# Kernel tuning notes

Hardware: AMD Instinct MI355X
Metric: run time of the kernel (lower is better)

The kernel has to match this reference:

```python
import jax, jax.numpy as jnp
import numpy as np

N_NODES = 25000
N_EDGES = 250000
DIM = 64
HEADS = 4
BN_EPS = 1e-5


def setup_inputs() -> dict:
    key = jax.random.key(0)
    ks = jax.random.split(key, 6)
    x = jax.random.normal(ks[0], (N_NODES, DIM), dtype=jnp.float32)
    edge_index = jax.random.randint(ks[1], (2, N_EDGES), 0, N_NODES)
    edge_attr = jax.random.normal(ks[2], (N_EDGES, DIM), dtype=jnp.float32)
    # learned params of GATGNN_AGAT_LAYER (xavier-ish scale)
    W = jax.random.normal(ks[3], (2 * DIM, HEADS * DIM), dtype=jnp.float32) * 0.05
    att = jax.random.normal(ks[4], (1, HEADS, 2 * DIM), dtype=jnp.float32) * 0.05
    bias = jnp.zeros((DIM,), dtype=jnp.float32)
    # BatchNorm1d(heads) in eval mode (running stats)
    bn_gamma = jnp.ones((HEADS,), dtype=jnp.float32)
    bn_beta = jnp.zeros((HEADS,), dtype=jnp.float32)
    bn_mean = jnp.zeros((HEADS,), dtype=jnp.float32)
    bn_var = jnp.ones((HEADS,), dtype=jnp.float32)
    return {"x": x, "edge_attr": edge_attr, "W": W, "att": att, "bias": bias,
            "bn_gamma": bn_gamma, "bn_beta": bn_beta, "bn_mean": bn_mean,
            "bn_var": bn_var, "edge_index": edge_index}


def reference(x, edge_attr, W, att, bias, bn_gamma, bn_beta, bn_mean, bn_var, edge_index):
    act = jax.nn.softplus  # act='softplus' in DSDCrystal
    # flow='target_to_source': i = edge_index[0] (aggregation index), j = edge_index[1]
    idx_i = edge_index[0]
    idx_j = edge_index[1]
    x_i = x[idx_i]                                   # [E, D] gather
    x_j = x[idx_j]                                   # [E, D] gather
    out_i = act(jnp.concatenate([x_i, edge_attr], axis=-1) @ W)  # [E, H*D]
    out_j = act(jnp.concatenate([x_j, edge_attr], axis=-1) @ W)  # [E, H*D]
    out_i = out_i.reshape(-1, HEADS, DIM)            # [E, H, D]
    out_j = out_j.reshape(-1, HEADS, DIM)
    # multi-head attention logits
    alpha = act(jnp.sum(jnp.concatenate([out_i, out_j], axis=-1) * att, axis=-1))  # [E, H]
    # BatchNorm1d(heads), eval mode
    alpha = act((alpha - bn_mean) / jnp.sqrt(bn_var + BN_EPS) * bn_gamma + bn_beta)
    # segment softmax over edges sharing the same target node i
    amax = jax.ops.segment_max(alpha, idx_i, num_segments=N_NODES)  # [N, H]
    e = jnp.exp(alpha - amax[idx_i])
    denom = jax.ops.segment_sum(e, idx_i, num_segments=N_NODES)[idx_i]  # [E, H]
    alpha = e / denom
    # weighted messages, scatter-add aggregation (dropout p=0.0 / eval)
    msg = out_j * alpha[:, :, None]                  # [E, H, D]
    aggr = jax.ops.segment_sum(msg, idx_i, num_segments=N_NODES)  # [N, H, D]
    # update: mean over heads + bias
    return aggr.mean(axis=1) + bias                  # [N, D]
```

## Files before the change

### kernel.cpp

```cpp
#include <hip/hip_runtime.h>
#include <hip/hip_bf16.h>
#include <math.h>

#define NN 25000
#define NE 250000
#define DD 64
#define HH 4
#define NGROUP (NE / 16)
#define NB 98

typedef __attribute__((ext_vector_type(8))) short bf16x8;
typedef __attribute__((ext_vector_type(4))) float f32x4;

#define WT_LD 136

__device__ __forceinline__ float softplus_f(float x) {
    return fmaxf(x, 0.0f) + __logf(1.0f + __expf(-fabsf(x)));
}

__device__ __forceinline__ unsigned short f2bf(float f) {
    __hip_bfloat16 h = __float2bfloat16(f);
    unsigned short u;
    __builtin_memcpy(&u, &h, 2);
    return u;
}

__device__ __forceinline__ float bf2f(unsigned short u) {
    return __uint_as_float(((unsigned int)u) << 16);
}

__device__ __forceinline__ void load8(const float* p, bf16x8& hi, bf16x8& lo) {
    float4 a = *(const float4*)p;
    float4 b = *(const float4*)(p + 4);
    float v[8] = {a.x, a.y, a.z, a.w, b.x, b.y, b.z, b.w};
#pragma unroll
    for (int i = 0; i < 8; ++i) {
        unsigned short h = f2bf(v[i]);
        hi[i] = (short)h;
        lo[i] = (short)f2bf(v[i] - bf2f(h));
    }
}

__global__ __launch_bounds__(512, 4)
void k_edge(const float* __restrict__ x, const float* __restrict__ ea,
            const float* __restrict__ W, const float* __restrict__ att,
            const float* __restrict__ bn_g, const float* __restrict__ bn_b,
            const float* __restrict__ bn_m, const float* __restrict__ bn_v,
            const int* __restrict__ eidx,
            unsigned short* __restrict__ outj,
            float* __restrict__ expa, float* __restrict__ denom)
{
    __shared__ unsigned short Wsh[256 * WT_LD];
    __shared__ float attI[256], attJ[256];

    const int tid = threadIdx.x;
    const int lane = tid & 63;
    const int q = lane >> 4;
    const int r = lane & 15;

    for (int idx = tid; idx < 32768; idx += 512) {
        int k = idx >> 8, n = idx & 255;
        Wsh[n * WT_LD + k] = f2bf(W[idx]);
    }
    if (tid < 256) {
        int c = tid;
        attI[c] = att[(c >> 6) * 128 + (c & 63)];
        attJ[c] = att[(c >> 6) * 128 + 64 + (c & 63)];
    }
    float bnsc[HH], bnsh[HH];
#pragma unroll
    for (int t = 0; t < HH; ++t) {
        float inv = rsqrtf(bn_v[t] + 1e-5f);
        bnsc[t] = bn_g[t] * inv;
        bnsh[t] = bn_b[t] - bn_m[t] * bn_g[t] * inv;
    }
    __syncthreads();

    const int gw = blockIdx.x * 8 + (tid >> 6);
    const int nw = gridDim.x * 8;

    for (int g = gw; g < NGROUP; g += nw) {
        const int e0 = g * 16;
        const int ei = eidx[e0 + r];
        const int ej = eidx[NE + e0 + r];
        const float* xi = x + (size_t)ei * DD;
        const float* xj = x + (size_t)ej * DD;
        const float* ev = ea + (size_t)(e0 + r) * DD;

        bf16x8 Ahi[6], Alo[6];
        load8(xi + q * 8,      Ahi[0], Alo[0]);
        load8(xi + 32 + q * 8, Ahi[1], Alo[1]);
        load8(xj + q * 8,      Ahi[2], Alo[2]);
        load8(xj + 32 + q * 8, Ahi[3], Alo[3]);
        load8(ev + q * 8,      Ahi[4], Alo[4]);
        load8(ev + 32 + q * 8, Ahi[5], Alo[5]);

        float lg[4][4];
#pragma unroll
        for (int a = 0; a < 4; ++a)
#pragma unroll
            for (int b = 0; b < 4; ++b) lg[a][b] = 0.f;

#pragma unroll
        for (int nt = 0; nt < 4; ++nt) {
            f32x4 ai[4], aj[4];
#pragma unroll
            for (int h = 0; h < 4; ++h) {
                ai[h] = (f32x4){0.f, 0.f, 0.f, 0.f};
                aj[h] = (f32x4){0.f, 0.f, 0.f, 0.f};
            }
#pragma unroll
            for (int h = 0; h < 4; ++h) {
                const unsigned short* bp = &Wsh[((nt + 4 * h) * 16 + r) * WT_LD + q * 8];
#pragma unroll
                for (int kt = 0; kt < 4; ++kt) {
                    bf16x8 bf = *(const bf16x8*)(bp + kt * 32);
                    const int fi = (kt < 2) ? kt : kt + 2;
                    const int fj = kt + 2;
                    ai[h] = __builtin_amdgcn_mfma_f32_16x16x32_bf16(Ahi[fi], bf, ai[h], 0, 0, 0);
                    ai[h] = __builtin_amdgcn_mfma_f32_16x16x32_bf16(Alo[fi], bf, ai[h], 0, 0, 0);
                    aj[h] = __builtin_amdgcn_mfma_f32_16x16x32_bf16(Ahi[fj], bf, aj[h], 0, 0, 0);
                    aj[h] = __builtin_amdgcn_mfma_f32_16x16x32_bf16(Alo[fj], bf, aj[h], 0, 0, 0);
                }
            }
            const int dbase = nt * 16 + r;
#pragma unroll
            for (int reg = 0; reg < 4; ++reg) {
                ushort4 pk;
                unsigned short* pkp = (unsigned short*)&pk;
#pragma unroll
                for (int h = 0; h < 4; ++h) {
                    const int c = dbase + 64 * h;
                    float spi = softplus_f(ai[h][reg]);
                    float spj = softplus_f(aj[h][reg]);
                    lg[reg][h] += spi * attI[c] + spj * attJ[c];
                    pkp[h] = f2bf(spj);
                }
                const unsigned e = (unsigned)(e0 + q * 4 + reg);
                *(ushort4*)&outj[e * 256 + dbase * 4] = pk;
            }
        }

#pragma unroll
        for (int off = 1; off < 16; off <<= 1) {
#pragma unroll
            for (int a = 0; a < 4; ++a)
#pragma unroll
                for (int b = 0; b < 4; ++b)
                    lg[a][b] += __shfl_xor(lg[a][b], off, 64);
        }
        float exv[4][4];
#pragma unroll
        for (int reg = 0; reg < 4; ++reg)
#pragma unroll
            for (int h = 0; h < 4; ++h)
                exv[reg][h] = __expf(softplus_f(fmaf(lg[reg][h], bnsc[h], bnsh[h])));

        if (r < 4) {
#pragma unroll
            for (int reg = 0; reg < 4; ++reg) {
                const int e = e0 + q * 4 + reg;
                const int ii = eidx[e];
                expa[e * 4 + r] = exv[reg][r];
                atomicAdd(&denom[ii * 4 + r], exv[reg][r]);
            }
        }
    }
}

__global__ __launch_bounds__(256)
void k_hist(const int* __restrict__ eidx, int* __restrict__ cnt) {
    const int e = blockIdx.x * 256 + threadIdx.x;
    if (e < NE) atomicAdd(&cnt[eidx[e]], 1);
}

__global__ __launch_bounds__(256)
void k_scanA(const int* __restrict__ cnt, int* __restrict__ offs,
             int* __restrict__ bsum) {
    __shared__ int s[256];
    const int tid = threadIdx.x;
    const int i = blockIdx.x * 256 + tid;
    int v = (i < NN) ? cnt[i] : 0;
    s[tid] = v;
    __syncthreads();
#pragma unroll
    for (int off = 1; off < 256; off <<= 1) {
        int t = (tid >= off) ? s[tid - off] : 0;
        __syncthreads();
        s[tid] += t;
        __syncthreads();
    }
    if (i < NN) offs[i] = s[tid] - v;
    if (tid == 255) bsum[blockIdx.x] = s[255];
}

__global__ __launch_bounds__(128)
void k_scanB(const int* __restrict__ bsum, int* __restrict__ bbase) {
    __shared__ int s[128];
    const int tid = threadIdx.x;
    int v = (tid < NB) ? bsum[tid] : 0;
    s[tid] = v;
    __syncthreads();
#pragma unroll
    for (int off = 1; off < 128; off <<= 1) {
        int t = (tid >= off) ? s[tid - off] : 0;
        __syncthreads();
        s[tid] += t;
        __syncthreads();
    }
    if (tid < NB) bbase[tid] = s[tid] - v;
}

__global__ __launch_bounds__(256)
void k_scanC(int* __restrict__ offs, const int* __restrict__ bbase,
             int* __restrict__ cursor) {
    const int i = blockIdx.x * 256 + threadIdx.x;
    if (i < NN) {
        const int o = offs[i] + bbase[blockIdx.x];
        offs[i] = o;
        cursor[i] = o;
    }
    if (i == 0) offs[NN] = NE;
}

__global__ __launch_bounds__(256)
void k_place(const int* __restrict__ eidx, int* __restrict__ cursor,
             int* __restrict__ perm) {
    const int e = blockIdx.x * 256 + threadIdx.x;
    if (e < NE) {
        const int pos = atomicAdd(&cursor[eidx[e]], 1);
        perm[pos] = e;
    }
}

__global__ __launch_bounds__(256)
void k_aggr(const int* __restrict__ offs, const int* __restrict__ perm,
            const unsigned short* __restrict__ outj,
            const float* __restrict__ expa,
            const float* __restrict__ denom,
            const float* __restrict__ bias,
            float* __restrict__ out)
{
    const int n = blockIdx.x * 4 + (threadIdx.x >> 6);
    if (n >= NN) return;
    const int lane = threadIdx.x & 63;
    const int k0 = offs[n], k1 = offs[n + 1];
    const float4 dv = *(const float4*)&denom[n * 4];
    float num0 = 0.f, num1 = 0.f, num2 = 0.f, num3 = 0.f;

    if (k0 < k1) {
        int e = perm[k0];
        float4 ex = *(const float4*)&expa[e * 4];
        ushort4 v = *(const ushort4*)&outj[((unsigned)e << 8) | (lane << 2)];
        for (int k = k0; k < k1; ++k) {
            float4 exc = ex; ushort4 vc = v;
            if (k + 1 < k1) {
                const int e2 = perm[k + 1];
                ex = *(const float4*)&expa[e2 * 4];
                v  = *(const ushort4*)&outj[((unsigned)e2 << 8) | (lane << 2)];
            }
            num0 += exc.x * bf2f(vc.x);
            num1 += exc.y * bf2f(vc.y);
            num2 += exc.z * bf2f(vc.z);
            num3 += exc.w * bf2f(vc.w);
        }
    }
    float r = 0.f;
    r += (dv.x > 0.f) ? num0 / dv.x : 0.f;
    r += (dv.y > 0.f) ? num1 / dv.y : 0.f;
    r += (dv.z > 0.f) ? num2 / dv.z : 0.f;
    r += (dv.w > 0.f) ? num3 / dv.w : 0.f;
    out[n * DD + lane] = 0.25f * r + bias[lane];
}

extern "C" void kernel_launch(void* const* d_in, const int* in_sizes, int n_in,
                              void* d_out, int out_size, void* d_ws, size_t ws_size,
                              hipStream_t stream)
{
    (void)in_sizes; (void)n_in; (void)out_size; (void)ws_size;
    const float* x    = (const float*)d_in[0];
    const float* ea   = (const float*)d_in[1];
    const float* W    = (const float*)d_in[2];
    const float* att  = (const float*)d_in[3];
    const float* bias = (const float*)d_in[4];
    const float* bn_g = (const float*)d_in[5];
    const float* bn_b = (const float*)d_in[6];
    const float* bn_m = (const float*)d_in[7];
    const float* bn_v = (const float*)d_in[8];
    const int*   eidx = (const int*)d_in[9];
    float* out = (float*)d_out;

    char* ws = (char*)d_ws;
    unsigned short* outj = (unsigned short*)ws;
    float* expa  = (float*)(ws + (size_t)NE * 512);
    float* denom = (float*)(ws + (size_t)NE * 512 + (size_t)NE * 16);
    int*   cnt    = (int*)(denom + (size_t)NN * 4);
    int*   offs   = cnt + NN;
    int*   cursor = offs + NN + 1;
    int*   perm   = cursor + NN;
    int*   bsum   = perm + NE;
    int*   bbase  = bsum + NB;

    hipMemsetAsync(denom, 0, (size_t)NN * 5 * sizeof(int), stream);

    k_hist <<<dim3((NE + 255) / 256), dim3(256), 0, stream>>>(eidx, cnt);
    k_scanA<<<dim3(NB), dim3(256), 0, stream>>>(cnt, offs, bsum);
    k_scanB<<<dim3(1), dim3(128), 0, stream>>>(bsum, bbase);
    k_scanC<<<dim3(NB), dim3(256), 0, stream>>>(offs, bbase, cursor);
    k_place<<<dim3((NE + 255) / 256), dim3(256), 0, stream>>>(eidx, cursor, perm);

    k_edge<<<dim3(512), dim3(512), 0, stream>>>(
        x, ea, W, att, bn_g, bn_b, bn_m, bn_v, eidx, outj, expa, denom);

    k_aggr<<<dim3((NN + 3) / 4), dim3(256), 0, stream>>>(
        offs, perm, outj, expa, denom, bias, out);
}
```

Measured before the change: 323.3 us.

## Process edges in sorted order so aggregation reads contiguous outputs

The edge kernel now walks edges through the CSR permutation and writes outj and expa at the sorted position. The aggregation kernel can then stream a contiguous range per node without indirect perm lookups, and its manual prefetch is dropped. The cost moves into the edge kernel, which now gathers edge_attr rows in permuted, random order instead of reading them sequentially. Target indices for the denominator atomics are taken by shuffle instead of a reload.

```diff
diff --git a/kernel.cpp b/kernel.cpp
--- a/kernel.cpp
+++ b/kernel.cpp
@@ -46,7 +46,7 @@
             const float* __restrict__ W, const float* __restrict__ att,
             const float* __restrict__ bn_g, const float* __restrict__ bn_b,
             const float* __restrict__ bn_m, const float* __restrict__ bn_v,
-            const int* __restrict__ eidx,
+            const int* __restrict__ eidx, const int* __restrict__ perm,
             unsigned short* __restrict__ outj,
             float* __restrict__ expa, float* __restrict__ denom)
 {
@@ -81,11 +81,12 @@
 
     for (int g = gw; g < NGROUP; g += nw) {
         const int e0 = g * 16;
-        const int ei = eidx[e0 + r];
-        const int ej = eidx[NE + e0 + r];
+        const int pe = perm[e0 + r];
+        const int ei = eidx[pe];
+        const int ej = eidx[NE + pe];
         const float* xi = x + (size_t)ei * DD;
         const float* xj = x + (size_t)ej * DD;
-        const float* ev = ea + (size_t)(e0 + r) * DD;
+        const float* ev = ea + (size_t)pe * DD;
 
         bf16x8 Ahi[6], Alo[6];
         load8(xi + q * 8,      Ahi[0], Alo[0]);
@@ -136,8 +137,8 @@
                     lg[reg][h] += spi * attI[c] + spj * attJ[c];
                     pkp[h] = f2bf(spj);
                 }
-                const unsigned e = (unsigned)(e0 + q * 4 + reg);
-                *(ushort4*)&outj[e * 256 + dbase * 4] = pk;
+                const unsigned p = (unsigned)(e0 + q * 4 + reg);
+                *(ushort4*)&outj[p * 256 + dbase * 4] = pk;
             }
         }
 
@@ -156,13 +157,17 @@
             for (int h = 0; h < 4; ++h)
                 exv[reg][h] = __expf(softplus_f(fmaf(lg[reg][h], bnsc[h], bnsh[h])));
 
+        int iis[4];
+#pragma unroll
+        for (int reg = 0; reg < 4; ++reg)
+            iis[reg] = __shfl(ei, q * 4 + reg, 16);
+
         if (r < 4) {
 #pragma unroll
             for (int reg = 0; reg < 4; ++reg) {
-                const int e = e0 + q * 4 + reg;
-                const int ii = eidx[e];
-                expa[e * 4 + r] = exv[reg][r];
-                atomicAdd(&denom[ii * 4 + r], exv[reg][r]);
+                const int p = e0 + q * 4 + reg;
+                expa[p * 4 + r] = exv[reg][r];
+                atomicAdd(&denom[iis[reg] * 4 + r], exv[reg][r]);
             }
         }
     }
@@ -234,7 +239,7 @@
 }
 
 __global__ __launch_bounds__(256)
-void k_aggr(const int* __restrict__ offs, const int* __restrict__ perm,
+void k_aggr(const int* __restrict__ offs,
             const unsigned short* __restrict__ outj,
             const float* __restrict__ expa,
             const float* __restrict__ denom,
@@ -247,23 +252,13 @@
     const int k0 = offs[n], k1 = offs[n + 1];
     const float4 dv = *(const float4*)&denom[n * 4];
     float num0 = 0.f, num1 = 0.f, num2 = 0.f, num3 = 0.f;
-
-    if (k0 < k1) {
-        int e = perm[k0];
-        float4 ex = *(const float4*)&expa[e * 4];
-        ushort4 v = *(const ushort4*)&outj[((unsigned)e << 8) | (lane << 2)];
-        for (int k = k0; k < k1; ++k) {
-            float4 exc = ex; ushort4 vc = v;
-            if (k + 1 < k1) {
-                const int e2 = perm[k + 1];
-                ex = *(const float4*)&expa[e2 * 4];
-                v  = *(const ushort4*)&outj[((unsigned)e2 << 8) | (lane << 2)];
-            }
-            num0 += exc.x * bf2f(vc.x);
-            num1 += exc.y * bf2f(vc.y);
-            num2 += exc.z * bf2f(vc.z);
-            num3 += exc.w * bf2f(vc.w);
-        }
+    for (int k = k0; k < k1; ++k) {
+        const float4 ex = *(const float4*)&expa[k * 4];
+        const ushort4 v = *(const ushort4*)&outj[((unsigned)k << 8) | (lane << 2)];
+        num0 += ex.x * bf2f(v.x);
+        num1 += ex.y * bf2f(v.y);
+        num2 += ex.z * bf2f(v.z);
+        num3 += ex.w * bf2f(v.w);
     }
     float r = 0.f;
     r += (dv.x > 0.f) ? num0 / dv.x : 0.f;
@@ -310,8 +305,8 @@
     k_place<<<dim3((NE + 255) / 256), dim3(256), 0, stream>>>(eidx, cursor, perm);
 
     k_edge<<<dim3(512), dim3(512), 0, stream>>>(
-        x, ea, W, att, bn_g, bn_b, bn_m, bn_v, eidx, outj, expa, denom);
+        x, ea, W, att, bn_g, bn_b, bn_m, bn_v, eidx, perm, outj, expa, denom);
 
     k_aggr<<<dim3((NN + 3) / 4), dim3(256), 0, stream>>>(
-        offs, perm, outj, expa, denom, bias, out);
-}
+        offs, outj, expa, denom, bias, out);
+}
```

After: 321.1 us. No clear change (-0.7%).
